# Kernel optimization log

Hardware: AMD Instinct MI355X
Metric: run time of the kernel (lower is better)

## Reference

```python
import jax, jax.numpy as jnp
import numpy as np

C, N, G = 10, 500000, 8


def setup_inputs() -> dict:
    key = jax.random.key(0)
    k1, k2 = jax.random.split(key)
    group_act = jax.random.uniform(k1, (C, N, G), dtype=jnp.float32)
    target_labels = jax.random.randint(k2, (N,), 0, 11, dtype=jnp.int64 if jax.config.jax_enable_x64 else jnp.int32)
    return {"group_act": group_act, "target_labels": target_labels}


def reference(group_act, target_labels):
    # group_act: [C, N, G] (stacked list_group_activation), target_labels: [N] in 0..C (0 => ignored)
    labels = target_labels.reshape(-1) - 1                      # [N], -1 => skip
    c, n, g = group_act.shape
    masks = (labels[None, :] == jnp.arange(c)[:, None]).astype(group_act.dtype)  # [C, N]
    counts = masks.sum(axis=1)                                  # [C]
    valid = counts >= 2                                         # classes actually contributing

    Am = group_act * masks[:, :, None]                          # [C, N, G] masked activations
    col_sum = Am.sum(axis=1)                                    # [C, G]
    p = Am / col_sum[:, None, :]                                # normalized per column (zero on unmasked rows)
    # log only over masked rows (original indexes rows by cls_mask before log)
    m3 = masks[:, :, None] > 0
    logp = jnp.where(m3, jnp.log(jnp.where(m3, p, 1.0)), 0.0)   # [C, N, G]

    # M[c, i, j] = sum_n p[c,n,i] * log p[c,n,j]; loss_ij = -M[c,i,j] for i != j
    M = jnp.einsum('cni,cnj->cij', p, logp)                     # [C, G, G]
    offdiag = M * (1.0 - jnp.eye(g, dtype=M.dtype))
    per_class = offdiag.sum(axis=(1, 2))                        # [C]

    num = jnp.sum(jnp.where(valid, per_class, 0.0))
    denom = jnp.sum(valid.astype(M.dtype)) * (g * (g - 1))
    # original: tot = mean(-M_ij); return -tot == mean(M_ij)
    return num / denom
```

## Files before the change

kernel.cpp:

```cpp
#include <hip/hip_runtime.h>

#define C_CLS 10
#define G_DIM 8
#define CHUNKS 128
#define ACC_W 26

__global__ void k_init(float* acc) {
    int t = threadIdx.x;
    if (t < C_CLS * ACC_W) acc[t] = 0.0f;
}

__device__ inline float wave_red(float v) {
#pragma unroll
    for (int off = 32; off > 0; off >>= 1) v += __shfl_down(v, off, 64);
    return v;
}

__global__ void __launch_bounds__(256) k_main(const float* __restrict__ ga,
                                              const int* __restrict__ lbl,
                                              float* __restrict__ g_acc, int N) {
    const int c = blockIdx.y;
    const int chunk_len = (N + CHUNKS - 1) / CHUNKS;
    const int base = blockIdx.x * chunk_len;
    const int end = min(base + chunk_len, N);

    float cs_a[G_DIM], R_a[G_DIM], D_a[G_DIM];
#pragma unroll
    for (int g = 0; g < G_DIM; ++g) { cs_a[g] = 0.0f; R_a[g] = 0.0f; D_a[g] = 0.0f; }
    float cnt = 0.0f;

    const float* plane = ga + (size_t)c * N * G_DIM;
    for (int n = base + (int)threadIdx.x; n < end; n += blockDim.x) {
        const float4* row = (const float4*)(plane + (size_t)n * G_DIM);
        float4 v0 = row[0];
        float4 v1 = row[1];
        int l = lbl[n];
        float m = (l == c + 1) ? 1.0f : 0.0f;
        float a[G_DIM] = {v0.x, v0.y, v0.z, v0.w, v1.x, v1.y, v1.z, v1.w};
        float la[G_DIM];
        float L = 0.0f;
#pragma unroll
        for (int g = 0; g < G_DIM; ++g) {
            la[g] = __logf(fmaxf(a[g], 1e-30f));
            L += la[g];
        }
        cnt += m;
#pragma unroll
        for (int g = 0; g < G_DIM; ++g) {
            float am = a[g] * m;
            cs_a[g] += am;
            R_a[g] = fmaf(am, L, R_a[g]);
            D_a[g] = fmaf(am, la[g], D_a[g]);
        }
    }

#pragma unroll
    for (int g = 0; g < G_DIM; ++g) {
        cs_a[g] = wave_red(cs_a[g]);
        R_a[g] = wave_red(R_a[g]);
        D_a[g] = wave_red(D_a[g]);
    }
    cnt = wave_red(cnt);

    __shared__ float s_part[4][ACC_W];
    int wid = threadIdx.x >> 6, lid = threadIdx.x & 63;
    if (lid == 0) {
#pragma unroll
        for (int g = 0; g < G_DIM; ++g) {
            s_part[wid][g] = cs_a[g];
            s_part[wid][8 + g] = R_a[g];
            s_part[wid][16 + g] = D_a[g];
        }
        s_part[wid][24] = cnt;
    }
    __syncthreads();
    int t = threadIdx.x;
    if (t < ACC_W - 1) {
        float v = s_part[0][t] + s_part[1][t] + s_part[2][t] + s_part[3][t];
        atomicAdd(&g_acc[c * ACC_W + t], v);
    }
}

__global__ void k_fin(const float* __restrict__ acc, float* __restrict__ out) {
    if (threadIdx.x == 0) {
        float tot = 0.0f;
        int nv = 0;
        for (int c = 0; c < C_CLS; ++c) {
            const float* a = acc + c * ACC_W;
            float cnt = a[24];
            if (cnt >= 2.0f) {
                nv++;
                float Lc = 0.0f, s = 0.0f;
                for (int i = 0; i < G_DIM; ++i) {
                    float cs = a[i];
                    Lc += __logf(cs);
                    s += (a[8 + i] - a[16 + i]) / cs;
                }
                tot += s - (float)(G_DIM - 1) * Lc;
            }
        }
        out[0] = tot / ((float)nv * (float)(G_DIM * (G_DIM - 1)));
    }
}

extern "C" void kernel_launch(void* const* d_in, const int* in_sizes, int n_in,
                              void* d_out, int out_size, void* d_ws, size_t ws_size,
                              hipStream_t stream) {
    const float* ga = (const float*)d_in[0];
    const int* lbl = (const int*)d_in[1];
    float* out = (float*)d_out;
    int N = in_sizes[1];

    float* acc = (float*)d_ws;

    k_init<<<1, 512, 0, stream>>>(acc);
    dim3 grid(CHUNKS, C_CLS);
    k_main<<<grid, 256, 0, stream>>>(ga, lbl, acc, N);
    k_fin<<<1, 64, 0, stream>>>(acc, out);
}
```

Before: 241.7 us.

## Load activation rows only for label-matching samples; replace atomics with per-block partials

Each thread now checks the label first and loads and processes the 32-byte activation row only when it belongs to the current class. Since roughly one row in eleven matches a given class, most of each class plane is no longer read from memory, and the log and accumulate work shrinks the same way. The zero-init kernel and global atomics are replaced by per-block partial sums written to the workspace. The final kernel then reduces those partials in parallel before computing the loss. The sparse, data-dependent loads add divergence and give uncoalesced access, but the kernel's cost was dominated by memory bandwidth.

Result: faster. 224.7 us (-7.0%).

```diff
diff --git a/kernel.cpp b/kernel.cpp
--- a/kernel.cpp
+++ b/kernel.cpp
@@ -3,12 +3,7 @@
 #define C_CLS 10
 #define G_DIM 8
 #define CHUNKS 128
-#define ACC_W 26
-
-__global__ void k_init(float* acc) {
-    int t = threadIdx.x;
-    if (t < C_CLS * ACC_W) acc[t] = 0.0f;
-}
+#define ACC_W 25
 
 __device__ inline float wave_red(float v) {
 #pragma unroll
@@ -18,47 +13,46 @@
 
 __global__ void __launch_bounds__(256) k_main(const float* __restrict__ ga,
                                               const int* __restrict__ lbl,
-                                              float* __restrict__ g_acc, int N) {
+                                              float* __restrict__ part, int N) {
     const int c = blockIdx.y;
     const int chunk_len = (N + CHUNKS - 1) / CHUNKS;
     const int base = blockIdx.x * chunk_len;
     const int end = min(base + chunk_len, N);
 
-    float cs_a[G_DIM], R_a[G_DIM], D_a[G_DIM];
-#pragma unroll
-    for (int g = 0; g < G_DIM; ++g) { cs_a[g] = 0.0f; R_a[g] = 0.0f; D_a[g] = 0.0f; }
+    float cs_a[G_DIM] = {0,0,0,0,0,0,0,0};
+    float R_a[G_DIM]  = {0,0,0,0,0,0,0,0};
+    float D_a[G_DIM]  = {0,0,0,0,0,0,0,0};
     float cnt = 0.0f;
 
     const float* plane = ga + (size_t)c * N * G_DIM;
     for (int n = base + (int)threadIdx.x; n < end; n += blockDim.x) {
-        const float4* row = (const float4*)(plane + (size_t)n * G_DIM);
-        float4 v0 = row[0];
-        float4 v1 = row[1];
-        int l = lbl[n];
-        float m = (l == c + 1) ? 1.0f : 0.0f;
-        float a[G_DIM] = {v0.x, v0.y, v0.z, v0.w, v1.x, v1.y, v1.z, v1.w};
-        float la[G_DIM];
-        float L = 0.0f;
+        if (lbl[n] == c + 1) {
+            const float4* row = (const float4*)(plane + (size_t)n * G_DIM);
+            float4 v0 = row[0];
+            float4 v1 = row[1];
+            float a[G_DIM] = {v0.x, v0.y, v0.z, v0.w, v1.x, v1.y, v1.z, v1.w};
+            float la[G_DIM];
+            float L = 0.0f;
 #pragma unroll
-        for (int g = 0; g < G_DIM; ++g) {
-            la[g] = __logf(fmaxf(a[g], 1e-30f));
-            L += la[g];
-        }
-        cnt += m;
+            for (int g = 0; g < G_DIM; ++g) {
+                la[g] = __logf(fmaxf(a[g], 1e-30f));
+                L += la[g];
+            }
+            cnt += 1.0f;
 #pragma unroll
-        for (int g = 0; g < G_DIM; ++g) {
-            float am = a[g] * m;
-            cs_a[g] += am;
-            R_a[g] = fmaf(am, L, R_a[g]);
-            D_a[g] = fmaf(am, la[g], D_a[g]);
+            for (int g = 0; g < G_DIM; ++g) {
+                cs_a[g] += a[g];
+                R_a[g] = fmaf(a[g], L, R_a[g]);
+                D_a[g] = fmaf(a[g], la[g], D_a[g]);
+            }
         }
     }
 
 #pragma unroll
     for (int g = 0; g < G_DIM; ++g) {
         cs_a[g] = wave_red(cs_a[g]);
-        R_a[g] = wave_red(R_a[g]);
-        D_a[g] = wave_red(D_a[g]);
+        R_a[g]  = wave_red(R_a[g]);
+        D_a[g]  = wave_red(D_a[g]);
     }
     cnt = wave_red(cnt);
 
@@ -67,36 +61,44 @@
     if (lid == 0) {
 #pragma unroll
         for (int g = 0; g < G_DIM; ++g) {
-            s_part[wid][g] = cs_a[g];
-            s_part[wid][8 + g] = R_a[g];
+            s_part[wid][g]      = cs_a[g];
+            s_part[wid][8 + g]  = R_a[g];
             s_part[wid][16 + g] = D_a[g];
         }
         s_part[wid][24] = cnt;
     }
     __syncthreads();
     int t = threadIdx.x;
-    if (t < ACC_W - 1) {
+    if (t < ACC_W) {
         float v = s_part[0][t] + s_part[1][t] + s_part[2][t] + s_part[3][t];
-        atomicAdd(&g_acc[c * ACC_W + t], v);
+        part[((size_t)c * CHUNKS + blockIdx.x) * ACC_W + t] = v;
     }
 }
 
-__global__ void k_fin(const float* __restrict__ acc, float* __restrict__ out) {
-    if (threadIdx.x == 0) {
+__global__ void k_fin(const float* __restrict__ part, float* __restrict__ out) {
+    __shared__ float s_acc[C_CLS][ACC_W];
+    int t = threadIdx.x;
+    if (t < C_CLS * ACC_W) {
+        int c = t / ACC_W, j = t % ACC_W;
+        float s = 0.0f;
+        for (int ch = 0; ch < CHUNKS; ++ch)
+            s += part[((size_t)c * CHUNKS + ch) * ACC_W + j];
+        s_acc[c][j] = s;
+    }
+    __syncthreads();
+    if (t == 0) {
         float tot = 0.0f;
         int nv = 0;
         for (int c = 0; c < C_CLS; ++c) {
-            const float* a = acc + c * ACC_W;
-            float cnt = a[24];
-            if (cnt >= 2.0f) {
+            if (s_acc[c][24] >= 2.0f) {
                 nv++;
-                float Lc = 0.0f, s = 0.0f;
+                float K = 0.0f, s = 0.0f;
                 for (int i = 0; i < G_DIM; ++i) {
-                    float cs = a[i];
-                    Lc += __logf(cs);
-                    s += (a[8 + i] - a[16 + i]) / cs;
+                    float cs = s_acc[c][i];
+                    K += __logf(cs);
+                    s += (s_acc[c][8 + i] - s_acc[c][16 + i]) / cs;
                 }
-                tot += s - (float)(G_DIM - 1) * Lc;
+                tot += s - (float)(G_DIM - 1) * K;
             }
         }
         out[0] = tot / ((float)nv * (float)(G_DIM * (G_DIM - 1)));
@@ -111,10 +113,9 @@
     float* out = (float*)d_out;
     int N = in_sizes[1];
 
-    float* acc = (float*)d_ws;
+    float* part = (float*)d_ws;
 
-    k_init<<<1, 512, 0, stream>>>(acc);
     dim3 grid(CHUNKS, C_CLS);
-    k_main<<<grid, 256, 0, stream>>>(ga, lbl, acc, N);
-    k_fin<<<1, 64, 0, stream>>>(acc, out);
+    k_main<<<grid, 256, 0, stream>>>(ga, lbl, part, N);
+    k_fin<<<1, 256, 0, stream>>>(part, out);
 }
```
